# Kernel optimization log

Measured on AMD Instinct MI355X. Metric: run time of the kernel, lower is better.

## Reference

```python
import jax, jax.numpy as jnp
import numpy as np

D_MODEL = 2048
MLP = 8192
E = 8
R = 16
ALPHA = 32
SCALING = ALPHA / R  # lora_alpha / rank


def setup_inputs() -> dict:
    key = jax.random.key(0)
    ks = jax.random.split(key, 16)
    s = 0.02
    return {
        "x": jax.random.normal(ks[0], (4, 1024, D_MODEL), dtype=jnp.float32),
        # frozen base weights (nn.Linear stores [out, in])
        "w_gate": jax.random.normal(ks[1], (MLP, D_MODEL), dtype=jnp.float32) * s,
        "w_up": jax.random.normal(ks[2], (MLP, D_MODEL), dtype=jnp.float32) * s,
        "w_down": jax.random.normal(ks[3], (D_MODEL, MLP), dtype=jnp.float32) * s,
        # router
        "router_w": jax.random.normal(ks[4], (E, D_MODEL), dtype=jnp.float32) * s,
        "router_b": jnp.zeros((E,), dtype=jnp.float32),
        # LoRA expert params: A [E, r, fan_in], B [E, fan_out, r]
        "A_gate": jax.random.normal(ks[5], (E, R, D_MODEL), dtype=jnp.float32) * s,
        "B_gate": jax.random.normal(ks[6], (E, MLP, R), dtype=jnp.float32) * s,
        "A_up": jax.random.normal(ks[7], (E, R, D_MODEL), dtype=jnp.float32) * s,
        "B_up": jax.random.normal(ks[8], (E, MLP, R), dtype=jnp.float32) * s,
        "A_down": jax.random.normal(ks[9], (E, R, MLP), dtype=jnp.float32) * s,
        "B_down": jax.random.normal(ks[10], (E, D_MODEL, R), dtype=jnp.float32) * s,
    }


def _lora_moe_sparse(inp, W, A, B, onehot):
    # inp: [B,S,din], W: [dout,din], A: [E,r,din], B: [E,dout,r], onehot: [B,S,E]
    base = jnp.einsum("bsd,od->bso", inp, W)
    # low-rank projection for every expert is tiny: [B,S,E,r]
    t = jnp.einsum("bsd,erd->bser", inp, A)
    # top-1 dispatch: onehot zeroes out non-selected experts (== scatter assign,
    # since each token has exactly one expert)
    lora = jnp.einsum("bser,bse,eor->bso", t, onehot, B) * SCALING
    return base + lora


def reference(x, w_gate, w_up, w_down, router_w, router_b,
              A_gate, B_gate, A_up, B_up, A_down, B_down):
    logits = jnp.einsum("bsd,ed->bse", x, router_w) + router_b
    routing = jax.nn.softmax(logits, axis=-1)
    index = jnp.argmax(routing, axis=-1)                 # [B,S]
    y_hard = jax.nn.one_hot(index, E, dtype=logits.dtype)  # [B,S,E]
    expert_choice = y_hard - jax.lax.stop_gradient(routing) + routing

    gate_out = _lora_moe_sparse(x, w_gate, A_gate, B_gate, y_hard)
    up_out = _lora_moe_sparse(x, w_up, A_up, B_up, y_hard)
    h = jax.nn.silu(gate_out) * up_out
    out = _lora_moe_sparse(h, w_down, A_down, B_down, y_hard)
    return (out, routing, expert_choice)
```

## Files before the change

kernel.cpp:

```cpp
#include <hip/hip_runtime.h>
#include <stdint.h>

#define NTOK   4096
#define DM     2048
#define DMLP   8192
#define NEXP   8
#define NRANK  16
#define SCAL   2.0f

#define LDXA 2304
#define LDHA 8320

typedef __bf16 bf16x8 __attribute__((ext_vector_type(8)));
typedef float  f32x4  __attribute__((ext_vector_type(4)));
typedef unsigned short u16;

__device__ __forceinline__ u16 f2bf(float f) {
  unsigned u = __float_as_uint(f);
  u += 0x7fffu + ((u >> 16) & 1u);
  return (u16)(u >> 16);
}

__device__ __forceinline__ void gload_lds16(const void* g, void* l) {
  __builtin_amdgcn_global_load_lds((const __attribute__((address_space(1))) void*)g,
                                   (__attribute__((address_space(3))) void*)l, 16, 0, 0);
}

__global__ void cvt_kernel(const float* __restrict__ src, u16* __restrict__ dst, int n4) {
  int i = blockIdx.x * blockDim.x + threadIdx.x;
  int stride = gridDim.x * blockDim.x;
  for (; i < n4; i += stride) {
    float4 v = ((const float4*)src)[i];
    ushort4 o;
    o.x = f2bf(v.x); o.y = f2bf(v.y); o.z = f2bf(v.z); o.w = f2bf(v.w);
    ((ushort4*)dst)[i] = o;
  }
}

__global__ void build_wx(const float* __restrict__ W,
                         const float* __restrict__ Bm,
                         u16* __restrict__ dst,
                         int din, int ldx, int extoff, int browstride) {
  const int o = blockIdx.x;
  const int tid = threadIdx.x;
  u16* drow = dst + (size_t)o * ldx;
  const float* wrow = W + (size_t)o * din;
  for (int c4 = tid; c4 < din / 4; c4 += 256) {
    float4 v = ((const float4*)wrow)[c4];
    ushort4 ov;
    ov.x = f2bf(v.x); ov.y = f2bf(v.y); ov.z = f2bf(v.z); ov.w = f2bf(v.w);
    ((ushort4*)drow)[c4] = ov;
  }
  const int next = ldx - din;
  if (tid < next) {
    int c = tid;
    u16 val = 0;
    if (c >= extoff && c < extoff + NEXP * NRANK) {
      int ce = c - extoff;
      int e = ce >> 4, r = ce & 15;
      val = f2bf(Bm[((size_t)e * browstride + o) * NRANK + r]);
    }
    drow[din + c] = val;
  }
}

__global__ void router_kernel(const float* __restrict__ x,
                              const float* __restrict__ rw,
                              const float* __restrict__ rb,
                              u16* __restrict__ xa,
                              int* __restrict__ idx,
                              float* __restrict__ out_rout,
                              float* __restrict__ out_ec) {
  const int wave = threadIdx.x >> 6;
  const int lane = threadIdx.x & 63;
  const int m = blockIdx.x * 4 + wave;

  const float4* xrow = (const float4*)(x + (size_t)m * DM + lane * 32);
  float4 xv[8];
#pragma unroll
  for (int i = 0; i < 8; ++i) xv[i] = xrow[i];

  uint4 o[4];
  unsigned* op = (unsigned*)o;
#pragma unroll
  for (int i = 0; i < 8; ++i) {
    op[2*i]   = (unsigned)f2bf(xv[i].x) | ((unsigned)f2bf(xv[i].y) << 16);
    op[2*i+1] = (unsigned)f2bf(xv[i].z) | ((unsigned)f2bf(xv[i].w) << 16);
  }
  uint4* xdst = (uint4*)(xa + (size_t)m * LDXA + lane * 32);
#pragma unroll
  for (int i = 0; i < 4; ++i) xdst[i] = o[i];

  float lg[NEXP];
#pragma unroll
  for (int e = 0; e < NEXP; ++e) {
    const float4* wrow = (const float4*)(rw + (size_t)e * DM + lane * 32);
    float s = 0.f;
#pragma unroll
    for (int i = 0; i < 8; ++i) {
      float4 wv = wrow[i];
      s += xv[i].x*wv.x + xv[i].y*wv.y + xv[i].z*wv.z + xv[i].w*wv.w;
    }
#pragma unroll
    for (int off = 32; off > 0; off >>= 1) s += __shfl_xor(s, off, 64);
    lg[e] = s + rb[e];
  }

  float mx = lg[0];
#pragma unroll
  for (int e = 1; e < NEXP; ++e) mx = fmaxf(mx, lg[e]);
  float ex[NEXP], se = 0.f;
#pragma unroll
  for (int e = 0; e < NEXP; ++e) { ex[e] = expf(lg[e] - mx); se += ex[e]; }
  float inv = 1.f / se;
  int best = 0; float bv = lg[0];
#pragma unroll
  for (int e = 1; e < NEXP; ++e) if (lg[e] > bv) { bv = lg[e]; best = e; }

  if (lane == 0) {
    idx[m] = best;
#pragma unroll
    for (int e = 0; e < NEXP; ++e) {
      float r = ex[e] * inv;
      out_rout[(size_t)m * NEXP + e] = r;
      float hard = (e == best) ? 1.f : 0.f;
      out_ec[(size_t)m * NEXP + e] = (hard - r) + r;
    }
  }
}

template<int MODE>
__global__ __launch_bounds__(256, 2)
void gemm_kernel(const u16* __restrict__ A,
                 const u16* __restrict__ B0,
                 const int* __restrict__ idx,
                 void* __restrict__ Cout)
{
  constexpr int LDA = (MODE == 0) ? LDXA : LDHA;
  constexpr int LDB = (MODE == 0) ? 2048 : 8192;
  constexpr int NKI = (MODE == 0) ? 64 : 32;

  __shared__ u16 lds[16384];

  const int tid = threadIdx.x;
  const int w = tid >> 6;
  const int l = tid & 63;
  const int wm = w >> 1, wn = w & 1;
  const int mtile = blockIdx.x;
  const int ntile = (MODE == 3) ? 0 : (int)blockIdx.y;
  const int ks    = (MODE == 3) ? (int)blockIdx.y : 0;
  const int kb0   = (MODE == 3) ? ks * 1024 : 0;

  int srow[2];
  srow[0] = w * 16 + (l >> 2);
  srow[1] = 64 + srow[0];
  const int chunk = (l & 3) ^ ((srow[0] >> 1) & 3);
  const int scol = chunk * 8;

  const u16* aptr[2];
  const u16* bptr[2];
#pragma unroll
  for (int i = 0; i < 2; ++i) {
    aptr[i] = A + (size_t)(mtile * 128 + srow[i]) * LDA + kb0 + scol;
    bptr[i] = B0 + (size_t)(ntile * 128 + srow[i]) * LDB + kb0 + scol;
  }

  char* ldsc = (char*)lds;
  auto stage = [&](int buf, int kt) {
    const int kk = kt * 32;
    char* base = ldsc + buf * 16384;
#pragma unroll
    for (int i = 0; i < 2; ++i) {
      gload_lds16(aptr[i] + kk, base + i * 4096 + w * 1024);
      gload_lds16(bptr[i] + kk, base + 8192 + i * 4096 + w * 1024);
    }
  };

  f32x4 acc[4][4];
  f32x4 zf = {0.f, 0.f, 0.f, 0.f};
#pragma unroll
  for (int a = 0; a < 4; ++a)
#pragma unroll
    for (int b = 0; b < 4; ++b) acc[a][b] = zf;

  stage(0, 0);
  __syncthreads();

  const int kq   = l >> 4;
  const int arow = wm * 64 + (l & 15);
  const int brow = wn * 64 + (l & 15);
  const int axor = (kq ^ ((arow >> 1) & 3)) << 4;
  const int bxor = (kq ^ ((brow >> 1) & 3)) << 4;

  for (int kt = 0; kt < NKI; ++kt) {
    const int buf = kt & 1;
    if (kt + 1 < NKI) stage(buf ^ 1, kt + 1);
    const char* bA = ldsc + buf * 16384;
    const char* bB = bA + 8192;
    bf16x8 af[4], bfr[4];
#pragma unroll
    for (int fm = 0; fm < 4; ++fm)
      af[fm] = *(const bf16x8*)(bA + (arow + fm * 16) * 64 + axor);
#pragma unroll
    for (int fn = 0; fn < 4; ++fn)
      bfr[fn] = *(const bf16x8*)(bB + (brow + fn * 16) * 64 + bxor);
#pragma unroll
    for (int fm = 0; fm < 4; ++fm)
#pragma unroll
      for (int fn = 0; fn < 4; ++fn)
        acc[fm][fn] = __builtin_amdgcn_mfma_f32_16x16x32_bf16(af[fm], bfr[fn], acc[fm][fn], 0, 0, 0);
    __syncthreads();
  }

  const int lq = l >> 4;
  const int lr = l & 15;

  if (MODE == 0) {
    u16* X = (u16*)Cout;
#pragma unroll
    for (int fm = 0; fm < 4; ++fm)
#pragma unroll
      for (int fn = 0; fn < 4; ++fn)
        for (int j = 0; j < 4; ++j) {
          int m = mtile * 128 + wm * 64 + fm * 16 + lq * 4 + j;
          int c = ntile * 128 + wn * 64 + fn * 16 + lr;
          int e = idx[m];
          u16 v = (((c & 127) >> 4) == e) ? f2bf(SCAL * acc[fm][fn][j]) : (u16)0;
          X[(size_t)m * LDXA + 2048 + c] = v;
        }
  } else {
    float* P = (float*)Cout + (size_t)ks * NTOK * 128;
#pragma unroll
    for (int fm = 0; fm < 4; ++fm)
#pragma unroll
      for (int fn = 0; fn < 4; ++fn)
        for (int j = 0; j < 4; ++j) {
          int m = mtile * 128 + wm * 64 + fm * 16 + lq * 4 + j;
          int c = wn * 64 + fn * 16 + lr;
          P[(size_t)m * 128 + c] = acc[fm][fn][j];
        }
  }
}

template<int BM, int NKT, int LDA, int LDB, int M8>
__global__ __launch_bounds__(512, 2)
void gemm8(const u16* __restrict__ Ag,
           const u16* __restrict__ B0g,
           const u16* __restrict__ B1g,
           void* __restrict__ Cout)
{
  constexpr int FM  = BM / 32;
  constexpr int FH  = FM / 2;
  constexpr int APL = BM / 128;
  constexpr int ASL = BM * 64;
  constexpr int NIT = NKT / 2;
  constexpr int NTILES = (M8 == 1) ? 64 : 8;
  constexpr int NWG    = (M8 == 1) ? 1024 : 256;

  __shared__ char lds8[4 * ASL + 65536];

  const int tid = threadIdx.x;
  const int w = tid >> 6, l = tid & 63;
  const int wm = w >> 2, wn = w & 3;

  const int bid = blockIdx.x;
  const int swz = (bid & 7) * (NWG / 8) + (bid >> 3);
  const int mtile = swz / NTILES;
  const int ntile = swz % NTILES;

  auto stage_a = [&](int buf, int s, int kt) {
    int ktc = kt < NKT - 1 ? kt : NKT - 1;
#pragma unroll
    for (int i = 0; i < APL; ++i) {
      int row = i * 128 + (tid >> 2);
      int lc  = (tid & 3) ^ ((row >> 1) & 3);
      const u16* g = Ag + (size_t)(mtile * BM + row) * LDA + ktc * 64 + s * 32 + lc * 8;
      char* lp = lds8 + (buf * 2 + s) * ASL + i * 8192 + w * 1024;
      gload_lds16(g, lp);
    }
  };
  auto stage_b = [&](int buf, int s, int kt) {
    int ktc = kt < NKT - 1 ? kt : NKT - 1;
#pragma unroll
    for (int i = 0; i < 2; ++i) {
      int row = i * 128 + (tid >> 2);
      int lc  = (tid & 3) ^ ((row >> 1) & 3);
      const u16* src;
      size_t roff;
      if (M8 == 1) {
        int c = ntile * 128 + ((row >> 5) << 4) + (row & 15);
        src = ((row >> 4) & 1) ? B1g : B0g;
        roff = (size_t)c * LDB;
      } else {
        src = B0g;
        roff = (size_t)(ntile * 256 + row) * LDB;
      }
      const u16* g = src + roff + ktc * 64 + s * 32 + lc * 8;
      char* lp = lds8 + 4 * ASL + (buf * 2 + s) * 16384 + i * 8192 + w * 1024;
      gload_lds16(g, lp);
    }
  };

  const int lr  = l & 15;
  const int kqp = l >> 4;
  const int ko  = ((kqp ^ ((lr >> 1) & 3)) << 4);

  bf16x8 a4[FH], b4[4];
  f32x4 acc[FM][4];
  f32x4 zf = {0.f, 0.f, 0.f, 0.f};
#pragma unroll
  for (int a = 0; a < FM; ++a)
#pragma unroll
    for (int b = 0; b < 4; ++b) acc[a][b] = zf;

  auto readA = [&](int buf, int s, int qa) {
#pragma unroll
    for (int f = 0; f < FH; ++f) {
      int row = wm * (BM / 2) + (qa * FH + f) * 16 + lr;
      a4[f] = *(const bf16x8*)(lds8 + (buf * 2 + s) * ASL + row * 64 + ko);
    }
  };
  auto readB = [&](int buf, int s) {
#pragma unroll
    for (int f = 0; f < 4; ++f) {
      int row = wn * 64 + f * 16 + lr;
      b4[f] = *(const bf16x8*)(lds8 + 4 * ASL + (buf * 2 + s) * 16384 + row * 64 + ko);
    }
  };
  auto waitvm = [&] {
    if constexpr (BM == 256) asm volatile("s_waitcnt vmcnt(8)" ::: "memory");
    else                     asm volatile("s_waitcnt vmcnt(6)" ::: "memory");
  };

#define MFMA_Q(qa) \
  _Pragma("unroll") \
  for (int f = 0; f < FH; ++f) \
    _Pragma("unroll") \
    for (int n = 0; n < 4; ++n) \
      acc[(qa) * FH + f][n] = \
        __builtin_amdgcn_mfma_f32_16x16x32_bf16(a4[f], b4[n], acc[(qa) * FH + f][n], 0, 0, 0);

#define PHASE(cb, s, qa, STG, doVM) \
  { if ((qa) == 0) readB(cb, s); \
    readA(cb, s, qa); \
    STG; \
    __builtin_amdgcn_sched_barrier(0); \
    __builtin_amdgcn_s_barrier(); \
    asm volatile("s_waitcnt lgkmcnt(0)" ::: "memory"); \
    __builtin_amdgcn_sched_barrier(0); \
    __builtin_amdgcn_s_setprio(1); \
    MFMA_Q(qa); \
    __builtin_amdgcn_s_setprio(0); \
    __builtin_amdgcn_sched_barrier(0); \
    if (doVM) { waitvm(); __builtin_amdgcn_sched_barrier(0); } \
    __builtin_amdgcn_s_barrier(); }

  stage_a(0, 0, 0); stage_b(0, 0, 0);
  stage_a(0, 1, 0); stage_b(0, 1, 0);
  stage_a(1, 0, 1); stage_b(1, 0, 1);
  waitvm();
  __builtin_amdgcn_sched_barrier(0);
  __builtin_amdgcn_s_barrier();

  for (int it = 0; it < NIT; ++it) {
    const int k1 = 2 * it + 1, k2 = 2 * it + 2, k3 = 2 * it + 3;
    PHASE(0, 0, 0, stage_a(1, 1, k1), 0)
    PHASE(0, 0, 1, stage_b(1, 1, k1), 1)
    PHASE(0, 1, 0, stage_a(0, 0, k2), 0)
    PHASE(0, 1, 1, stage_b(0, 0, k2), 1)
    PHASE(1, 0, 0, stage_a(0, 1, k2), 0)
    PHASE(1, 0, 1, stage_b(0, 1, k2), 1)
    PHASE(1, 1, 0, stage_a(1, 0, k3), 0)
    PHASE(1, 1, 1, stage_b(1, 0, k3), 1)
  }

  const int lq = l >> 4;
  if (M8 == 1) {
    u16* H = (u16*)Cout;
#pragma unroll
    for (int fm = 0; fm < FM; ++fm)
      for (int jj = 0; jj < 4; ++jj) {
        const int m = mtile * 256 + wm * 128 + fm * 16 + lq * 4 + jj;
#pragma unroll
        for (int p = 0; p < 2; ++p) {
          float g = acc[fm][2 * p][jj];
          float u = acc[fm][2 * p + 1][jj];
          float h = g / (1.f + __expf(-g)) * u;
          const int c = ntile * 128 + (wn * 2 + p) * 16 + lr;
          H[(size_t)m * LDHA + c] = f2bf(h);
        }
      }
  } else {
    float* C = (float*)Cout;
#pragma unroll
    for (int fm = 0; fm < FM; ++fm)
#pragma unroll
      for (int n = 0; n < 4; ++n)
        for (int jj = 0; jj < 4; ++jj) {
          const int m = mtile * 128 + wm * 64 + fm * 16 + lq * 4 + jj;
          const int c = ntile * 256 + wn * 64 + n * 16 + lr;
          C[(size_t)m * DM + c] = acc[fm][n][jj];
        }
  }
#undef PHASE
#undef MFMA_Q
}

__global__ void td_reduce(const float* __restrict__ part,
                          const int* __restrict__ idx,
                          u16* __restrict__ ha) {
  int i = blockIdx.x * blockDim.x + threadIdx.x;
  int m = i >> 7, c = i & 127;
  float s = 0.f;
#pragma unroll
  for (int k = 0; k < 8; ++k) s += part[(size_t)k * NTOK * 128 + i];
  u16 v = ((c >> 4) == idx[m]) ? f2bf(SCAL * s) : (u16)0;
  ha[(size_t)m * LDHA + 8192 + c] = v;
}

extern "C" void kernel_launch(void* const* d_in, const int* in_sizes, int n_in,
                              void* d_out, int out_size, void* d_ws, size_t ws_size,
                              hipStream_t stream) {
  const float* x  = (const float*)d_in[0];
  const float* wg = (const float*)d_in[1];
  const float* wu = (const float*)d_in[2];
  const float* wd = (const float*)d_in[3];
  const float* rw = (const float*)d_in[4];
  const float* rb = (const float*)d_in[5];
  const float* Ag = (const float*)d_in[6];
  const float* Bg = (const float*)d_in[7];
  const float* Au = (const float*)d_in[8];
  const float* Bu = (const float*)d_in[9];
  const float* Ad = (const float*)d_in[10];
  const float* Bd = (const float*)d_in[11];

  float* out      = (float*)d_out;
  float* out_rout = out + (size_t)NTOK * DM;
  float* out_ec   = out_rout + (size_t)NTOK * NEXP;

  char* ws = (char*)d_ws;
  size_t off = 0;
  auto take = [&](size_t b) { void* p = ws + off; off += (b + 255) & ~(size_t)255; return p; };
  u16*   xa   = (u16*)take((size_t)NTOK * LDXA * 2);
  u16*   ha   = (u16*)take((size_t)NTOK * LDHA * 2);
  u16*   wgx  = (u16*)take((size_t)DMLP * LDXA * 2);
  u16*   wux  = (u16*)take((size_t)DMLP * LDXA * 2);
  u16*   wdx  = (u16*)take((size_t)DM * LDHA * 2);
  u16*   Aab  = (u16*)take((size_t)256 * DM * 2);
  u16*   Adb  = (u16*)take((size_t)128 * DMLP * 2);
  float* tdp  = (float*)take((size_t)8 * NTOK * 128 * 4);
  int*   idx  = (int*)take((size_t)NTOK * 4);
  if (off > ws_size) return;

  cvt_kernel<<<64, 256, 0, stream>>>(Ag, Aab, 128 * DM / 4);
  cvt_kernel<<<64, 256, 0, stream>>>(Au, Aab + 128 * DM, 128 * DM / 4);
  cvt_kernel<<<128, 256, 0, stream>>>(Ad, Adb, 128 * DMLP / 4);

  build_wx<<<DMLP, 256, 0, stream>>>(wg, Bg, wgx, DM, LDXA, 0,   DMLP);
  build_wx<<<DMLP, 256, 0, stream>>>(wu, Bu, wux, DM, LDXA, 128, DMLP);
  build_wx<<<DM,   256, 0, stream>>>(wd, Bd, wdx, DMLP, LDHA, 0, DM);

  router_kernel<<<NTOK / 4, 256, 0, stream>>>(x, rw, rb, xa, idx, out_rout, out_ec);

  gemm_kernel<0><<<dim3(32, 2), 256, 0, stream>>>(xa, Aab, idx, xa);
  gemm8<256, 36, LDXA, LDXA, 1><<<1024, 512, 0, stream>>>(xa, wgx, wux, ha);
  gemm_kernel<3><<<dim3(32, 8), 256, 0, stream>>>(ha, Adb, idx, tdp);
  td_reduce<<<NTOK * 128 / 256, 256, 0, stream>>>(tdp, idx, ha);
  gemm8<128, 130, LDHA, LDHA, 2><<<256, 512, 0, stream>>>(ha, wdx, nullptr, out);
}
```

Before: 593.0 us.

## Restructure gemm8 pipeline: precomputed addresses, merged phases, new tile mapping

```diff
diff --git a/kernel.cpp b/kernel.cpp
--- a/kernel.cpp
+++ b/kernel.cpp
@@ -250,12 +250,10 @@
            void* __restrict__ Cout)
 {
   constexpr int FM  = BM / 32;
-  constexpr int FH  = FM / 2;
+  constexpr int QP  = (BM == 256) ? 2 : 1;
   constexpr int APL = BM / 128;
   constexpr int ASL = BM * 64;
   constexpr int NIT = NKT / 2;
-  constexpr int NTILES = (M8 == 1) ? 64 : 8;
-  constexpr int NWG    = (M8 == 1) ? 1024 : 256;
 
   __shared__ char lds8[4 * ASL + 65536];
 
@@ -264,48 +262,64 @@
   const int wm = w >> 2, wn = w & 3;
 
   const int bid = blockIdx.x;
-  const int swz = (bid & 7) * (NWG / 8) + (bid >> 3);
-  const int mtile = swz / NTILES;
-  const int ntile = swz % NTILES;
+  int mtile, ntile;
+  if (M8 == 1) {
+    int r = bid >> 3;
+    mtile = r >> 3;
+    ntile = (bid & 7) * 8 + (r & 7);
+  } else {
+    int swz = (bid & 7) * 32 + (bid >> 3);
+    mtile = swz >> 3;
+    ntile = swz & 7;
+  }
+
+  const u16* agb[APL];
+  const u16* bgb[2];
+#pragma unroll
+  for (int i = 0; i < APL; ++i) {
+    int row = i * 128 + (tid >> 2);
+    int lc  = (tid & 3) ^ ((row >> 1) & 3);
+    agb[i] = Ag + (size_t)(mtile * BM + row) * LDA + lc * 8;
+  }
+#pragma unroll
+  for (int i = 0; i < 2; ++i) {
+    int row = i * 128 + (tid >> 2);
+    int lc  = (tid & 3) ^ ((row >> 1) & 3);
+    if (M8 == 1) {
+      int c = ntile * 128 + ((row >> 5) << 4) + (row & 15);
+      bgb[i] = (((row >> 4) & 1) ? B1g : B0g) + (size_t)c * LDB + lc * 8;
+    } else {
+      bgb[i] = B0g + (size_t)(ntile * 256 + row) * LDB + lc * 8;
+    }
+  }
 
   auto stage_a = [&](int buf, int s, int kt) {
-    int ktc = kt < NKT - 1 ? kt : NKT - 1;
-#pragma unroll
-    for (int i = 0; i < APL; ++i) {
-      int row = i * 128 + (tid >> 2);
-      int lc  = (tid & 3) ^ ((row >> 1) & 3);
-      const u16* g = Ag + (size_t)(mtile * BM + row) * LDA + ktc * 64 + s * 32 + lc * 8;
-      char* lp = lds8 + (buf * 2 + s) * ASL + i * 8192 + w * 1024;
-      gload_lds16(g, lp);
-    }
+    const int ko = (kt < NKT - 1 ? kt : NKT - 1) * 64 + s * 32;
+#pragma unroll
+    for (int i = 0; i < APL; ++i)
+      gload_lds16(agb[i] + ko, lds8 + (buf * 2 + s) * ASL + i * 8192 + w * 1024);
   };
   auto stage_b = [&](int buf, int s, int kt) {
-    int ktc = kt < NKT - 1 ? kt : NKT - 1;
-#pragma unroll
-    for (int i = 0; i < 2; ++i) {
-      int row = i * 128 + (tid >> 2);
-      int lc  = (tid & 3) ^ ((row >> 1) & 3);
-      const u16* src;
-      size_t roff;
-      if (M8 == 1) {
-        int c = ntile * 128 + ((row >> 5) << 4) + (row & 15);
-        src = ((row >> 4) & 1) ? B1g : B0g;
-        roff = (size_t)c * LDB;
-      } else {
-        src = B0g;
-        roff = (size_t)(ntile * 256 + row) * LDB;
-      }
-      const u16* g = src + roff + ktc * 64 + s * 32 + lc * 8;
-      char* lp = lds8 + 4 * ASL + (buf * 2 + s) * 16384 + i * 8192 + w * 1024;
-      gload_lds16(g, lp);
-    }
+    const int ko = (kt < NKT - 1 ? kt : NKT - 1) * 64 + s * 32;
+#pragma unroll
+    for (int i = 0; i < 2; ++i)
+      gload_lds16(bgb[i] + ko, lds8 + 4 * ASL + (buf * 2 + s) * 16384 + i * 8192 + w * 1024);
   };
 
   const int lr  = l & 15;
-  const int kqp = l >> 4;
-  const int ko  = ((kqp ^ ((lr >> 1) & 3)) << 4);
-
-  bf16x8 a4[FH], b4[4];
+  const int kob = ((l >> 4) ^ ((lr >> 1) & 3)) << 4;
+  int aoff[QP][4];
+#pragma unroll
+  for (int qa = 0; qa < QP; ++qa)
+#pragma unroll
+    for (int f = 0; f < 4; ++f)
+      aoff[qa][f] = (wm * (BM / 2) + (qa * 4 + f) * 16 + lr) * 64 + kob;
+  int boff[4];
+#pragma unroll
+  for (int f = 0; f < 4; ++f)
+    boff[f] = (wn * 64 + f * 16 + lr) * 64 + kob;
+
+  bf16x8 a4[4], b4[4];
   f32x4 acc[FM][4];
   f32x4 zf = {0.f, 0.f, 0.f, 0.f};
 #pragma unroll
@@ -315,17 +329,13 @@
 
   auto readA = [&](int buf, int s, int qa) {
 #pragma unroll
-    for (int f = 0; f < FH; ++f) {
-      int row = wm * (BM / 2) + (qa * FH + f) * 16 + lr;
-      a4[f] = *(const bf16x8*)(lds8 + (buf * 2 + s) * ASL + row * 64 + ko);
-    }
+    for (int f = 0; f < 4; ++f)
+      a4[f] = *(const bf16x8*)(lds8 + (buf * 2 + s) * ASL + aoff[qa][f]);
   };
   auto readB = [&](int buf, int s) {
 #pragma unroll
-    for (int f = 0; f < 4; ++f) {
-      int row = wn * 64 + f * 16 + lr;
-      b4[f] = *(const bf16x8*)(lds8 + 4 * ASL + (buf * 2 + s) * 16384 + row * 64 + ko);
-    }
+    for (int f = 0; f < 4; ++f)
+      b4[f] = *(const bf16x8*)(lds8 + 4 * ASL + (buf * 2 + s) * 16384 + boff[f]);
   };
   auto waitvm = [&] {
     if constexpr (BM == 256) asm volatile("s_waitcnt vmcnt(8)" ::: "memory");
@@ -334,44 +344,55 @@
 
 #define MFMA_Q(qa) \
   _Pragma("unroll") \
-  for (int f = 0; f < FH; ++f) \
+  for (int f = 0; f < 4; ++f) \
     _Pragma("unroll") \
     for (int n = 0; n < 4; ++n) \
-      acc[(qa) * FH + f][n] = \
-        __builtin_amdgcn_mfma_f32_16x16x32_bf16(a4[f], b4[n], acc[(qa) * FH + f][n], 0, 0, 0);
+      acc[(qa) * 4 + f][n] = \
+        __builtin_amdgcn_mfma_f32_16x16x32_bf16(a4[f], b4[n], acc[(qa) * 4 + f][n], 0, 0, 0);
 
 #define PHASE(cb, s, qa, STG, doVM) \
-  { if ((qa) == 0) readB(cb, s); \
+  { STG; \
+    if ((qa) == 0) readB(cb, s); \
     readA(cb, s, qa); \
-    STG; \
-    __builtin_amdgcn_sched_barrier(0); \
     __builtin_amdgcn_s_barrier(); \
-    asm volatile("s_waitcnt lgkmcnt(0)" ::: "memory"); \
-    __builtin_amdgcn_sched_barrier(0); \
     __builtin_amdgcn_s_setprio(1); \
     MFMA_Q(qa); \
     __builtin_amdgcn_s_setprio(0); \
-    __builtin_amdgcn_sched_barrier(0); \
     if (doVM) { waitvm(); __builtin_amdgcn_sched_barrier(0); } \
     __builtin_amdgcn_s_barrier(); }
 
-  stage_a(0, 0, 0); stage_b(0, 0, 0);
-  stage_a(0, 1, 0); stage_b(0, 1, 0);
-  stage_a(1, 0, 1); stage_b(1, 0, 1);
-  waitvm();
-  __builtin_amdgcn_sched_barrier(0);
-  __builtin_amdgcn_s_barrier();
-
-  for (int it = 0; it < NIT; ++it) {
-    const int k1 = 2 * it + 1, k2 = 2 * it + 2, k3 = 2 * it + 3;
-    PHASE(0, 0, 0, stage_a(1, 1, k1), 0)
-    PHASE(0, 0, 1, stage_b(1, 1, k1), 1)
-    PHASE(0, 1, 0, stage_a(0, 0, k2), 0)
-    PHASE(0, 1, 1, stage_b(0, 0, k2), 1)
-    PHASE(1, 0, 0, stage_a(0, 1, k2), 0)
-    PHASE(1, 0, 1, stage_b(0, 1, k2), 1)
-    PHASE(1, 1, 0, stage_a(1, 0, k3), 0)
-    PHASE(1, 1, 1, stage_b(1, 0, k3), 1)
+  if constexpr (BM == 256) {
+    stage_a(0, 0, 0); stage_b(0, 0, 0);
+    stage_a(0, 1, 0); stage_b(0, 1, 0);
+    stage_a(1, 0, 1); stage_b(1, 0, 1);
+    waitvm();
+    __builtin_amdgcn_sched_barrier(0);
+    __builtin_amdgcn_s_barrier();
+    for (int it = 0; it < NIT; ++it) {
+      const int k1 = 2 * it + 1, k2 = 2 * it + 2, k3 = 2 * it + 3;
+      PHASE(0, 0, 0, stage_a(1, 1, k1), 0)
+      PHASE(0, 0, 1, stage_b(1, 1, k1), 1)
+      PHASE(0, 1, 0, stage_a(0, 0, k2), 0)
+      PHASE(0, 1, 1, stage_b(0, 0, k2), 1)
+      PHASE(1, 0, 0, stage_a(0, 1, k2), 0)
+      PHASE(1, 0, 1, stage_b(0, 1, k2), 1)
+      PHASE(1, 1, 0, stage_a(1, 0, k3), 0)
+      PHASE(1, 1, 1, stage_b(1, 0, k3), 1)
+    }
+  } else {
+    stage_a(0, 0, 0); stage_b(0, 0, 0);
+    stage_a(0, 1, 0); stage_b(0, 1, 0);
+    stage_a(1, 0, 1); stage_b(1, 0, 1);
+    waitvm();
+    __builtin_amdgcn_sched_barrier(0);
+    __builtin_amdgcn_s_barrier();
+    for (int it = 0; it < NIT; ++it) {
+      const int k1 = 2 * it + 1, k2 = 2 * it + 2, k3 = 2 * it + 3;
+      PHASE(0, 0, 0, { stage_a(1, 1, k1); stage_b(1, 1, k1); }, 1)
+      PHASE(0, 1, 0, { stage_a(0, 0, k2); stage_b(0, 0, k2); }, 1)
+      PHASE(1, 0, 0, { stage_a(0, 1, k2); stage_b(0, 1, k2); }, 1)
+      PHASE(1, 1, 0, { stage_a(1, 0, k3); stage_b(1, 0, k3); }, 1)
+    }
   }
 
   const int lq = l >> 4;
@@ -385,7 +406,8 @@
         for (int p = 0; p < 2; ++p) {
           float g = acc[fm][2 * p][jj];
           float u = acc[fm][2 * p + 1][jj];
-          float h = g / (1.f + __expf(-g)) * u;
+          float e = __builtin_amdgcn_exp2f(g * -1.44269504089f);
+          float h = g * __builtin_amdgcn_rcpf(1.f + e) * u;
           const int c = ntile * 128 + (wn * 2 + p) * 16 + lr;
           H[(size_t)m * LDHA + c] = f2bf(h);
         }
```

Result: faster. 574.7 us (-3.1%).
